# Performance work log

Measured on AMD Instinct MI355X. Metric: run time of the kernel, lower is better.

Reference implementation:

```python
import jax, jax.numpy as jnp
import numpy as np

CONF_TH = 0.25   # default conf_thresh in non_max_suppression
NMS_TH = 0.35    # default nms_thresh


def setup_inputs() -> dict:
    key = jax.random.key(0)
    # [N, C=5+num_classes, H, W]
    preds = jax.random.normal(key, (64, 85, 32, 32), dtype=jnp.float32)
    return {"preds": preds}


def _decode(preds):
    """Faithful box decode: [N,C,H,W] -> [N, H*W, 6] (x1,y1,x2,y2,score,cls)."""
    N, C, H, W = preds.shape
    p = jnp.transpose(preds, (0, 2, 3, 1))           # [N,H,W,C]
    pobj = p[..., 0]
    preg = p[..., 1:5]
    pcls = p[..., 5:]
    score = pobj * jnp.max(pcls, axis=-1)             # obj * max-class
    cls = jax.lax.stop_gradient(jnp.argmax(pcls, axis=-1).astype(preds.dtype))
    gy, gx = jnp.meshgrid(jnp.arange(H, dtype=preds.dtype),
                          jnp.arange(W, dtype=preds.dtype), indexing="ij")
    bw = jax.nn.sigmoid(preg[..., 2])
    bh = jax.nn.sigmoid(preg[..., 3])
    bcx = (jnp.tanh(preg[..., 0]) + gx) / W
    bcy = (jnp.tanh(preg[..., 1]) + gy) / H
    x1 = bcx - 0.5 * bw
    y1 = bcy - 0.5 * bh
    x2 = bcx + 0.5 * bw
    y2 = bcy + 0.5 * bh
    bboxes = jnp.stack([x1, y1, x2, y2, score, cls], axis=-1)  # [N,H,W,6]
    return bboxes.reshape(N, H * W, 6)


def _iou_matrix(boxes):
    """[M,4] xyxy -> [M,M] pairwise IoU."""
    x1, y1, x2, y2 = boxes[:, 0], boxes[:, 1], boxes[:, 2], boxes[:, 3]
    area = (x2 - x1) * (y2 - y1)
    iw = jnp.clip(jnp.minimum(x2[:, None], x2[None, :]) - jnp.maximum(x1[:, None], x1[None, :]), 0.0)
    ih = jnp.clip(jnp.minimum(y2[:, None], y2[None, :]) - jnp.maximum(y1[:, None], y1[None, :]), 0.0)
    inter = iw * ih
    return inter / (area[:, None] + area[None, :] - inter + 1e-9)


def _nms_single(bb):
    """Greedy class-aware NMS on one image's [M,6] boxes.
    Equivalent to: filter score>CONF_TH then torchvision.batched_nms.
    Returns keep mask [M] in the original box order (fixed shape)."""
    M = bb.shape[0]
    order = jnp.argsort(-bb[:, 4])                    # descending score
    b = bb[order]
    iou = _iou_matrix(b[:, :4])
    same_cls = b[:, 5][:, None] == b[:, 5][None, :]
    supp_mat = (iou > NMS_TH) & same_cls              # [M,M]
    valid_s = b[:, 4] > CONF_TH

    def body(i, keep):
        suppressed = jnp.any(keep & supp_mat[i])
        return keep.at[i].set(valid_s[i] & ~suppressed)

    keep_s = jax.lax.fori_loop(0, M, body, jnp.zeros((M,), jnp.bool_))
    # scatter back to original order
    return jnp.zeros((M,), jnp.bool_).at[order].set(keep_s)


def reference(preds):
    bboxes = _decode(preds)                # [N, HW, 6]
    keep = jax.vmap(_nms_single)(bboxes)   # [N, HW] bool keep mask
    return bboxes, keep
```

## Files before the change

### kernel.cpp

```cpp
#include <hip/hip_runtime.h>
#include <math.h>

#define NIMG 64
#define HW   1024
#define NCH  85
#define NCLS 80
#define CONF_TH 0.25f
#define NMS_TH  0.35f

__device__ __forceinline__ float fast_tanh(float x) {
  float e = __expf(2.0f * x);
  return 1.0f - 2.0f * __builtin_amdgcn_rcpf(e + 1.0f);
}
__device__ __forceinline__ float fast_sigmoid(float x) {
  return __builtin_amdgcn_rcpf(1.0f + __expf(-x));
}

template <int CL0, int NC>
__device__ __forceinline__ void quarter_argmax(const float* __restrict__ bp,
                                               float4& mv, int4& mi) {
  float4 v = *(const float4*)(bp + (size_t)CL0 * HW);
  float b0 = v.x, b1 = v.y, b2 = v.z, b3 = v.w;
  int i0 = CL0 - 5, i1 = i0, i2 = i0, i3 = i0;
#pragma unroll
  for (int c = 1; c < NC; ++c) {
    float4 u = *(const float4*)(bp + (size_t)(CL0 + c) * HW);
    int ci = CL0 - 5 + c;
    if (u.x > b0) { b0 = u.x; i0 = ci; }
    if (u.y > b1) { b1 = u.y; i1 = ci; }
    if (u.z > b2) { b2 = u.z; i2 = ci; }
    if (u.w > b3) { b3 = u.w; i3 = ci; }
  }
  mv = make_float4(b0, b1, b2, b3);
  mi = make_int4(i0, i1, i2, i3);
}

__global__ __launch_bounds__(1024) void fused_kernel(const float* __restrict__ preds,
                                                     float* __restrict__ out,
                                                     float* __restrict__ keepOut) {
  int n = blockIdx.x;
  int t = threadIdx.x;
  int q  = t >> 8;
  int pg = t & 255;

  __shared__ float sx1[HW], sy1[HW], sx2[HW], sy2[HW], sarea[HW], sscore[HW];
  __shared__ int scls[HW];
  __shared__ int bucket[HW];
  __shared__ int sorted[HW];
  __shared__ int srank[HW];
  __shared__ unsigned long long supp[HW];
  __shared__ int cnt[NCLS], offs[NCLS], start[NCLS];
  __shared__ float pmaxv[4][HW];
  __shared__ int   pmaxi[4][HW];
  __shared__ float sobj[HW];
  __shared__ float sreg[4][HW];

  if (t < NCLS) cnt[t] = 0;

  const float* bp = preds + (size_t)n * (NCH * HW) + 4 * pg;
  float4 mv; int4 mi;
  if (q == 0) {
    float4 vobj = *(const float4*)(bp);
    ((float4*)sobj)[pg] = vobj;
#pragma unroll
    for (int r = 0; r < 4; ++r) {
      float4 vr = *(const float4*)(bp + (size_t)(1 + r) * HW);
      ((float4*)&sreg[r][0])[pg] = vr;
    }
    quarter_argmax<5, 16>(bp, mv, mi);
  } else if (q == 1) {
    quarter_argmax<21, 21>(bp, mv, mi);
  } else if (q == 2) {
    quarter_argmax<42, 21>(bp, mv, mi);
  } else {
    quarter_argmax<63, 22>(bp, mv, mi);
  }
  ((float4*)&pmaxv[q][0])[pg] = mv;
  ((int4*)&pmaxi[q][0])[pg] = mi;
  __syncthreads();

  float pobj = sobj[t];
  float tx = sreg[0][t], ty = sreg[1][t], tw = sreg[2][t], th = sreg[3][t];
  float best = pmaxv[0][t]; int bc = pmaxi[0][t];
#pragma unroll
  for (int qq = 1; qq < 4; ++qq) {
    float v = pmaxv[qq][t];
    if (v > best) { best = v; bc = pmaxi[qq][t]; }
  }
  float score = pobj * best;

  float gx = (float)(t & 31);
  float gy = (float)(t >> 5);
  float bcx = (fast_tanh(tx) + gx) * 0.03125f;
  float bcy = (fast_tanh(ty) + gy) * 0.03125f;
  float bw = fast_sigmoid(tw);
  float bh = fast_sigmoid(th);

  float x1 = bcx - 0.5f * bw, y1 = bcy - 0.5f * bh;
  float x2 = bcx + 0.5f * bw, y2 = bcy + 0.5f * bh;

  size_t gb = (size_t)n * HW + t;
  float2* ob = (float2*)(out + gb * 6);
  ob[0] = make_float2(x1, y1);
  ob[1] = make_float2(x2, y2);
  ob[2] = make_float2(score, (float)bc);

  sx1[t] = x1; sy1[t] = y1; sx2[t] = x2; sy2[t] = y2;
  float aar = (x2 - x1) * (y2 - y1);
  sarea[t] = aar;
  sscore[t] = score;
  scls[t] = bc;
  bool valid = score > CONF_TH;
  keepOut[gb] = 0.0f;
  __syncthreads();

  if (valid) atomicAdd(&cnt[bc], 1);
  __syncthreads();

  if (t < 64) {
    int c0 = (2 * t < NCLS) ? cnt[2 * t] : 0;
    int c1 = (2 * t + 1 < NCLS) ? cnt[2 * t + 1] : 0;
    int ps = c0 + c1;
    int x = ps;
#pragma unroll
    for (int d = 1; d < 64; d <<= 1) {
      int y = __shfl_up(x, d, 64);
      if (t >= d) x += y;
    }
    int excl = x - ps;
    if (2 * t < NCLS)     { start[2 * t] = excl;          offs[2 * t] = excl; }
    if (2 * t + 1 < NCLS) { start[2 * t + 1] = excl + c0; offs[2 * t + 1] = excl + c0; }
  }
  __syncthreads();

  if (valid) {
    int p = atomicAdd(&offs[bc], 1);
    bucket[p] = t;
  }
  __syncthreads();

  if (valid) {
    int s0 = start[bc], m = cnt[bc];
    int r = 0;
    for (int j = 0; j < m; ++j) {
      int jb = bucket[s0 + j];
      float sj = sscore[jb];
      r += (sj > score) || (sj == score && jb < t);
    }
    srank[t] = r;
    sorted[s0 + r] = t;
  }
  __syncthreads();

  if (valid) {
    int s0 = start[bc];
    int a = srank[t];
    int lim = a < 64 ? a : 64;
    unsigned long long mask = 0ull;
    for (int b = 0; b < lim; ++b) {
      int jb = sorted[s0 + b];
      float iw = fminf(x2, sx2[jb]) - fmaxf(x1, sx1[jb]);
      float ih = fminf(y2, sy2[jb]) - fmaxf(y1, sy1[jb]);
      iw = fmaxf(iw, 0.0f);
      ih = fmaxf(ih, 0.0f);
      float inter = iw * ih;
      float iou = inter / (aar + sarea[jb] - inter + 1e-9f);
      if (iou > NMS_TH) mask |= (1ull << b);
    }
    supp[s0 + a] = mask;
  }
  __syncthreads();

  if (t < NCLS) {
    int m = cnt[t], s0 = start[t];
    if (m <= 64) {
      unsigned long long kept = 0ull;
      for (int a = 0; a < m; ++a) {
        unsigned long long sa = supp[s0 + a];
        if ((sa & kept) == 0ull) {
          kept |= (1ull << a);
          keepOut[(size_t)n * HW + sorted[s0 + a]] = 1.0f;
        }
      }
    } else {
      for (int a = 0; a < m; ++a) {
        int ia = sorted[s0 + a];
        float ax1 = sx1[ia], ay1 = sy1[ia], ax2 = sx2[ia], ay2 = sy2[ia];
        float ar2 = sarea[ia];
        bool kp = true;
        for (int b = 0; b < a; ++b) {
          if (!bucket[s0 + b]) continue;
          int jb = sorted[s0 + b];
          float iw = fminf(ax2, sx2[jb]) - fmaxf(ax1, sx1[jb]);
          float ih = fminf(ay2, sy2[jb]) - fmaxf(ay1, sy1[jb]);
          iw = fmaxf(iw, 0.0f);
          ih = fmaxf(ih, 0.0f);
          float inter = iw * ih;
          float iou = inter / (ar2 + sarea[jb] - inter + 1e-9f);
          if (iou > NMS_TH) { kp = false; break; }
        }
        bucket[s0 + a] = kp ? 1 : 0;
        if (kp) keepOut[(size_t)n * HW + ia] = 1.0f;
      }
    }
  }
}

extern "C" void kernel_launch(void* const* d_in, const int* in_sizes, int n_in,
                              void* d_out, int out_size, void* d_ws, size_t ws_size,
                              hipStream_t stream) {
  const float* preds = (const float*)d_in[0];
  float* out = (float*)d_out;
  float* keepOut = out + (size_t)NIMG * HW * 6;

  fused_kernel<<<NIMG, HW, 0, stream>>>(preds, out, keepOut);
}
```

Baseline: 74.24 us.

## Split fused decode+NMS into a grid-wide decode kernel and a per-image NMS kernel

```diff
diff --git a/kernel.cpp b/kernel.cpp
--- a/kernel.cpp
+++ b/kernel.cpp
@@ -16,32 +16,63 @@
   return __builtin_amdgcn_rcpf(1.0f + __expf(-x));
 }
 
-template <int CL0, int NC>
-__device__ __forceinline__ void quarter_argmax(const float* __restrict__ bp,
-                                               float4& mv, int4& mi) {
-  float4 v = *(const float4*)(bp + (size_t)CL0 * HW);
-  float b0 = v.x, b1 = v.y, b2 = v.z, b3 = v.w;
-  int i0 = CL0 - 5, i1 = i0, i2 = i0, i3 = i0;
+__global__ __launch_bounds__(256) void decode_kernel(const float* __restrict__ preds,
+                                                     float* __restrict__ out) {
+  int gid = blockIdx.x * 256 + threadIdx.x;
+  int n = gid >> 10;
+  int t = gid & 1023;
+  const float* bp = preds + (size_t)n * (NCH * HW) + t;
+
+  float pobj = bp[0];
+  float tx = bp[(size_t)1 * HW];
+  float ty = bp[(size_t)2 * HW];
+  float tw = bp[(size_t)3 * HW];
+  float th = bp[(size_t)4 * HW];
+
+  float b0, b1, b2, b3;
+  int i0, i1, i2, i3;
+  b0 = bp[(size_t)(5 +  0) * HW]; i0 =  0;
+  b1 = bp[(size_t)(5 + 20) * HW]; i1 = 20;
+  b2 = bp[(size_t)(5 + 40) * HW]; i2 = 40;
+  b3 = bp[(size_t)(5 + 60) * HW]; i3 = 60;
 #pragma unroll
-  for (int c = 1; c < NC; ++c) {
-    float4 u = *(const float4*)(bp + (size_t)(CL0 + c) * HW);
-    int ci = CL0 - 5 + c;
-    if (u.x > b0) { b0 = u.x; i0 = ci; }
-    if (u.y > b1) { b1 = u.y; i1 = ci; }
-    if (u.z > b2) { b2 = u.z; i2 = ci; }
-    if (u.w > b3) { b3 = u.w; i3 = ci; }
-  }
-  mv = make_float4(b0, b1, b2, b3);
-  mi = make_int4(i0, i1, i2, i3);
-}
-
-__global__ __launch_bounds__(1024) void fused_kernel(const float* __restrict__ preds,
-                                                     float* __restrict__ out,
-                                                     float* __restrict__ keepOut) {
+  for (int c = 1; c < 20; ++c) {
+    float v0 = bp[(size_t)(5 +  0 + c) * HW];
+    float v1 = bp[(size_t)(5 + 20 + c) * HW];
+    float v2 = bp[(size_t)(5 + 40 + c) * HW];
+    float v3 = bp[(size_t)(5 + 60 + c) * HW];
+    if (v0 > b0) { b0 = v0; i0 =  0 + c; }
+    if (v1 > b1) { b1 = v1; i1 = 20 + c; }
+    if (v2 > b2) { b2 = v2; i2 = 40 + c; }
+    if (v3 > b3) { b3 = v3; i3 = 60 + c; }
+  }
+  float best = b0; int bc = i0;
+  if (b1 > best) { best = b1; bc = i1; }
+  if (b2 > best) { best = b2; bc = i2; }
+  if (b3 > best) { best = b3; bc = i3; }
+
+  float score = pobj * best;
+
+  float gx = (float)(t & 31);
+  float gy = (float)(t >> 5);
+  float bcx = (fast_tanh(tx) + gx) * 0.03125f;
+  float bcy = (fast_tanh(ty) + gy) * 0.03125f;
+  float bw = fast_sigmoid(tw);
+  float bh = fast_sigmoid(th);
+
+  float x1 = bcx - 0.5f * bw, y1 = bcy - 0.5f * bh;
+  float x2 = bcx + 0.5f * bw, y2 = bcy + 0.5f * bh;
+
+  float2* ob = (float2*)(out + (size_t)gid * 6);
+  ob[0] = make_float2(x1, y1);
+  ob[1] = make_float2(x2, y2);
+  ob[2] = make_float2(score, (float)bc);
+}
+
+__global__ __launch_bounds__(1024) void nms_kernel(const float* __restrict__ boxes,
+                                                   float* __restrict__ keepOut) {
   int n = blockIdx.x;
   int t = threadIdx.x;
-  int q  = t >> 8;
-  int pg = t & 255;
 
   __shared__ float sx1[HW], sy1[HW], sx2[HW], sy2[HW], sarea[HW], sscore[HW];
   __shared__ int scls[HW];
@@ -50,63 +81,20 @@
   __shared__ int srank[HW];
   __shared__ unsigned long long supp[HW];
   __shared__ int cnt[NCLS], offs[NCLS], start[NCLS];
-  __shared__ float pmaxv[4][HW];
-  __shared__ int   pmaxi[4][HW];
-  __shared__ float sobj[HW];
-  __shared__ float sreg[4][HW];
 
   if (t < NCLS) cnt[t] = 0;
 
-  const float* bp = preds + (size_t)n * (NCH * HW) + 4 * pg;
-  float4 mv; int4 mi;
-  if (q == 0) {
-    float4 vobj = *(const float4*)(bp);
-    ((float4*)sobj)[pg] = vobj;
-#pragma unroll
-    for (int r = 0; r < 4; ++r) {
-      float4 vr = *(const float4*)(bp + (size_t)(1 + r) * HW);
-      ((float4*)&sreg[r][0])[pg] = vr;
-    }
-    quarter_argmax<5, 16>(bp, mv, mi);
-  } else if (q == 1) {
-    quarter_argmax<21, 21>(bp, mv, mi);
-  } else if (q == 2) {
-    quarter_argmax<42, 21>(bp, mv, mi);
-  } else {
-    quarter_argmax<63, 22>(bp, mv, mi);
-  }
-  ((float4*)&pmaxv[q][0])[pg] = mv;
-  ((int4*)&pmaxi[q][0])[pg] = mi;
-  __syncthreads();
-
-  float pobj = sobj[t];
-  float tx = sreg[0][t], ty = sreg[1][t], tw = sreg[2][t], th = sreg[3][t];
-  float best = pmaxv[0][t]; int bc = pmaxi[0][t];
-#pragma unroll
-  for (int qq = 1; qq < 4; ++qq) {
-    float v = pmaxv[qq][t];
-    if (v > best) { best = v; bc = pmaxi[qq][t]; }
-  }
-  float score = pobj * best;
-
-  float gx = (float)(t & 31);
-  float gy = (float)(t >> 5);
-  float bcx = (fast_tanh(tx) + gx) * 0.03125f;
-  float bcy = (fast_tanh(ty) + gy) * 0.03125f;
-  float bw = fast_sigmoid(tw);
-  float bh = fast_sigmoid(th);
-
-  float x1 = bcx - 0.5f * bw, y1 = bcy - 0.5f * bh;
-  float x2 = bcx + 0.5f * bw, y2 = bcy + 0.5f * bh;
-
   size_t gb = (size_t)n * HW + t;
-  float2* ob = (float2*)(out + gb * 6);
-  ob[0] = make_float2(x1, y1);
-  ob[1] = make_float2(x2, y2);
-  ob[2] = make_float2(score, (float)bc);
-
+  const float2* ib = (const float2*)(boxes + gb * 6);
+  float2 a01 = ib[0];
+  float2 a23 = ib[1];
+  float2 a45 = ib[2];
+  float x1 = a01.x, y1 = a01.y, x2 = a23.x, y2 = a23.y;
+  float score = a45.x;
+  int bc = (int)a45.y;
+
+  float aar = (x2 - x1) * (y2 - y1);
   sx1[t] = x1; sy1[t] = y1; sx2[t] = x2; sy2[t] = y2;
-  float aar = (x2 - x1) * (y2 - y1);
   sarea[t] = aar;
   sscore[t] = score;
   scls[t] = bc;
@@ -213,5 +201,6 @@
   float* out = (float*)d_out;
   float* keepOut = out + (size_t)NIMG * HW * 6;
 
-  fused_kernel<<<NIMG, HW, 0, stream>>>(preds, out, keepOut);
-}
+  decode_kernel<<<NIMG * HW / 256, 256, 0, stream>>>(preds, out);
+  nms_kernel<<<NIMG, HW, 0, stream>>>(out, keepOut);
+}
```

After: 73.85 us. Within noise of the previous version (-0.5%).

## Assign classes to wavefronts and run per-class NMS with ballot-based suppression

Applied to the files above, without the earlier changes.

```diff
diff --git a/kernel.cpp b/kernel.cpp
--- a/kernel.cpp
+++ b/kernel.cpp
@@ -5,6 +5,8 @@
 #define HW   1024
 #define NCH  85
 #define NCLS 80
+#define NW   16
+#define CPW  5
 #define CONF_TH 0.25f
 #define NMS_TH  0.35f
 
@@ -42,20 +44,18 @@
   int t = threadIdx.x;
   int q  = t >> 8;
   int pg = t & 255;
+  int wv   = t >> 6;
+  int lane = t & 63;
 
   __shared__ float sx1[HW], sy1[HW], sx2[HW], sy2[HW], sarea[HW], sscore[HW];
   __shared__ int scls[HW];
-  __shared__ int bucket[HW];
-  __shared__ int sorted[HW];
-  __shared__ int srank[HW];
-  __shared__ unsigned long long supp[HW];
-  __shared__ int cnt[NCLS], offs[NCLS], start[NCLS];
   __shared__ float pmaxv[4][HW];
   __shared__ int   pmaxi[4][HW];
   __shared__ float sobj[HW];
   __shared__ float sreg[4][HW];
-
-  if (t < NCLS) cnt[t] = 0;
+  __shared__ unsigned short mlist[NW][HW];
+  __shared__ unsigned short ssort[NW][64];
+  __shared__ unsigned long long wflags[NW][32];
 
   const float* bp = preds + (size_t)n * (NCH * HW) + 4 * pg;
   float4 mv; int4 mi;
@@ -106,101 +106,107 @@
   ob[2] = make_float2(score, (float)bc);
 
   sx1[t] = x1; sy1[t] = y1; sx2[t] = x2; sy2[t] = y2;
-  float aar = (x2 - x1) * (y2 - y1);
-  sarea[t] = aar;
+  sarea[t] = (x2 - x1) * (y2 - y1);
   sscore[t] = score;
   scls[t] = bc;
-  bool valid = score > CONF_TH;
   keepOut[gb] = 0.0f;
   __syncthreads();
 
-  if (valid) atomicAdd(&cnt[bc], 1);
-  __syncthreads();
-
-  if (t < 64) {
-    int c0 = (2 * t < NCLS) ? cnt[2 * t] : 0;
-    int c1 = (2 * t + 1 < NCLS) ? cnt[2 * t + 1] : 0;
-    int ps = c0 + c1;
-    int x = ps;
-#pragma unroll
-    for (int d = 1; d < 64; d <<= 1) {
-      int y = __shfl_up(x, d, 64);
-      if (t >= d) x += y;
+  int   cls_r[16];
+  float sc_r[16];
+#pragma unroll
+  for (int k = 0; k < 16; ++k) {
+    int p = (k << 6) | lane;
+    cls_r[k] = scls[p];
+    sc_r[k]  = sscore[p];
+  }
+
+  for (int ci = 0; ci < CPW; ++ci) {
+    int c = wv * CPW + ci;
+
+    int m = 0;
+#pragma unroll
+    for (int k = 0; k < 16; ++k) {
+      bool pred = (cls_r[k] == c) && (sc_r[k] > CONF_TH);
+      unsigned long long mask = __ballot(pred);
+      while (mask) {
+        int l = __ffsll((unsigned long long)mask) - 1;
+        mask &= mask - 1;
+        if (lane == 0) mlist[wv][m] = (unsigned short)((k << 6) | l);
+        ++m;
+      }
     }
-    int excl = x - ps;
-    if (2 * t < NCLS)     { start[2 * t] = excl;          offs[2 * t] = excl; }
-    if (2 * t + 1 < NCLS) { start[2 * t + 1] = excl + c0; offs[2 * t + 1] = excl + c0; }
-  }
-  __syncthreads();
-
-  if (valid) {
-    int p = atomicAdd(&offs[bc], 1);
-    bucket[p] = t;
-  }
-  __syncthreads();
-
-  if (valid) {
-    int s0 = start[bc], m = cnt[bc];
-    int r = 0;
-    for (int j = 0; j < m; ++j) {
-      int jb = bucket[s0 + j];
-      float sj = sscore[jb];
-      r += (sj > score) || (sj == score && jb < t);
-    }
-    srank[t] = r;
-    sorted[s0 + r] = t;
-  }
-  __syncthreads();
-
-  if (valid) {
-    int s0 = start[bc];
-    int a = srank[t];
-    int lim = a < 64 ? a : 64;
-    unsigned long long mask = 0ull;
-    for (int b = 0; b < lim; ++b) {
-      int jb = sorted[s0 + b];
-      float iw = fminf(x2, sx2[jb]) - fmaxf(x1, sx1[jb]);
-      float ih = fminf(y2, sy2[jb]) - fmaxf(y1, sy1[jb]);
-      iw = fmaxf(iw, 0.0f);
-      ih = fmaxf(ih, 0.0f);
-      float inter = iw * ih;
-      float iou = inter / (aar + sarea[jb] - inter + 1e-9f);
-      if (iou > NMS_TH) mask |= (1ull << b);
-    }
-    supp[s0 + a] = mask;
-  }
-  __syncthreads();
-
-  if (t < NCLS) {
-    int m = cnt[t], s0 = start[t];
+    if (m == 0) continue;
+
     if (m <= 64) {
+      int pj = 0; float scj = 0.0f; int rj = 0;
+      bool active = (lane < m);
+      if (active) { pj = mlist[wv][lane]; scj = sscore[pj]; }
+      for (int i = 0; i < m; ++i) {
+        int pi = mlist[wv][i];
+        float si = sscore[pi];
+        if (active) rj += (si > scj) || (si == scj && pi < pj);
+      }
+      if (active) ssort[wv][rj] = (unsigned short)pj;
+
+      float kx1 = 0, ky1 = 0, kx2 = 0, ky2 = 0, kar = 0;
+      if (active) {
+        int qb = ssort[wv][lane];
+        kx1 = sx1[qb]; ky1 = sy1[qb]; kx2 = sx2[qb]; ky2 = sy2[qb]; kar = sarea[qb];
+      }
+
       unsigned long long kept = 0ull;
       for (int a = 0; a < m; ++a) {
-        unsigned long long sa = supp[s0 + a];
-        if ((sa & kept) == 0ull) {
-          kept |= (1ull << a);
-          keepOut[(size_t)n * HW + sorted[s0 + a]] = 1.0f;
-        }
-      }
-    } else {
-      for (int a = 0; a < m; ++a) {
-        int ia = sorted[s0 + a];
-        float ax1 = sx1[ia], ay1 = sy1[ia], ax2 = sx2[ia], ay2 = sy2[ia];
-        float ar2 = sarea[ia];
-        bool kp = true;
-        for (int b = 0; b < a; ++b) {
-          if (!bucket[s0 + b]) continue;
-          int jb = sorted[s0 + b];
-          float iw = fminf(ax2, sx2[jb]) - fmaxf(ax1, sx1[jb]);
-          float ih = fminf(ay2, sy2[jb]) - fmaxf(ay1, sy1[jb]);
+        int qa = ssort[wv][a];
+        float ax1 = sx1[qa], ay1 = sy1[qa], ax2 = sx2[qa], ay2 = sy2[qa];
+        float aar = sarea[qa];
+        bool sup = false;
+        if (lane < a && ((kept >> lane) & 1ull)) {
+          float iw = fminf(ax2, kx2) - fmaxf(ax1, kx1);
+          float ih = fminf(ay2, ky2) - fmaxf(ay1, ky1);
           iw = fmaxf(iw, 0.0f);
           ih = fmaxf(ih, 0.0f);
           float inter = iw * ih;
-          float iou = inter / (ar2 + sarea[jb] - inter + 1e-9f);
-          if (iou > NMS_TH) { kp = false; break; }
+          float iou = inter / (aar + kar - inter + 1e-9f);
+          sup = iou > NMS_TH;
         }
-        bucket[s0 + a] = kp ? 1 : 0;
-        if (kp) keepOut[(size_t)n * HW + ia] = 1.0f;
+        unsigned long long v = __ballot(sup);
+        if (v == 0ull) {
+          kept |= (1ull << a);
+          if (lane == 0) keepOut[(size_t)n * HW + qa] = 1.0f;
+        }
+      }
+    } else {
+      if (lane == 0) {
+        for (int i = 0; i < 32; ++i) wflags[wv][i] = 0ull;
+        for (int a = 0; a < m; ++a) {
+          int bj = -1; float bs = 0.0f; int bpx = 0;
+          for (int j = 0; j < m; ++j) {
+            if ((wflags[wv][j >> 6] >> (j & 63)) & 1ull) continue;
+            int pj2 = mlist[wv][j];
+            float sj2 = sscore[pj2];
+            if (bj < 0 || sj2 > bs || (sj2 == bs && pj2 < bpx)) { bj = j; bs = sj2; bpx = pj2; }
+          }
+          wflags[wv][bj >> 6] |= 1ull << (bj & 63);
+          float cx1 = sx1[bpx], cy1 = sy1[bpx], cx2 = sx2[bpx], cy2 = sy2[bpx];
+          float car = sarea[bpx];
+          bool kp = true;
+          for (int j = 0; j < m && kp; ++j) {
+            if (!((wflags[wv][16 + (j >> 6)] >> (j & 63)) & 1ull)) continue;
+            int pj2 = mlist[wv][j];
+            float iw = fminf(cx2, sx2[pj2]) - fmaxf(cx1, sx1[pj2]);
+            float ih = fminf(cy2, sy2[pj2]) - fmaxf(cy1, sy1[pj2]);
+            iw = fmaxf(iw, 0.0f);
+            ih = fmaxf(ih, 0.0f);
+            float inter = iw * ih;
+            float iou = inter / (car + sarea[pj2] - inter + 1e-9f);
+            if (iou > NMS_TH) kp = false;
+          }
+          if (kp) {
+            wflags[wv][16 + (bj >> 6)] |= 1ull << (bj & 63);
+            keepOut[(size_t)n * HW + bpx] = 1.0f;
+          }
+        }
       }
     }
   }
```

Result: slower. 86.51 us (+16.5%).
